# Performance work log

Measured on AMD Instinct MI355X. Metric: run time of the kernel, lower is better.

The kernel has to match this reference:

```python
import jax, jax.numpy as jnp
import numpy as np

N, E, F_IN, H, D, HID, G = 50000, 800000, 64, 4, 32, 128, 1024
NEG_SLOPE = 0.2


def setup_inputs():
    key = jax.random.key(0)
    ks = jax.random.split(key, 32)
    inp = {
        "x": jax.random.normal(ks[0], (N, F_IN), dtype=jnp.float32),
        "edge_index": jax.random.randint(ks[1], (2, E), 0, N, dtype=jnp.int64),
        "batch": jnp.sort(jax.random.randint(ks[2], (N,), 0, G, dtype=jnp.int64)),
    }
    dims = [F_IN, HID, HID]
    i = 3
    for l, din in enumerate(dims):
        s = 1.0 / np.sqrt(din)
        inp[f"Wl{l}"] = jax.random.normal(ks[i], (din, H * D), dtype=jnp.float32) * s; i += 1
        inp[f"bl{l}"] = jnp.zeros((H * D,), dtype=jnp.float32)
        inp[f"Wr{l}"] = jax.random.normal(ks[i], (din, H * D), dtype=jnp.float32) * s; i += 1
        inp[f"br{l}"] = jnp.zeros((H * D,), dtype=jnp.float32)
        inp[f"att{l}"] = jax.random.normal(ks[i], (H, D), dtype=jnp.float32) * (1.0 / np.sqrt(D)); i += 1
        inp[f"b{l}"] = jnp.zeros((H * D,), dtype=jnp.float32)
    inp["Wh"] = jax.random.normal(ks[i], (HID, 1), dtype=jnp.float32) * (1.0 / np.sqrt(HID))
    inp["bh"] = jnp.zeros((1,), dtype=jnp.float32)
    return inp


def gatv2_layer(x, src, dst, Wl, bl, Wr, br, att, b):
    # GATv2Conv (eval mode, no dropout): e_ij = att . leaky_relu(Wl x_j + Wr x_i)
    xl = (x @ Wl + bl).reshape(-1, H, D)   # source transform
    xr = (x @ Wr + br).reshape(-1, H, D)   # target transform
    m = xl[src] + xr[dst]                  # [E,H,D]
    e = jnp.where(m >= 0, m, NEG_SLOPE * m)
    score = jnp.einsum("ehd,hd->eh", e, att)          # [E,H]
    smax = jax.ops.segment_max(score, dst, num_segments=N)  # [N,H]
    expv = jnp.exp(score - smax[dst])
    denom = jax.ops.segment_sum(expv, dst, num_segments=N)
    alpha = expv / denom[dst]                          # softmax over in-edges of dst
    agg = jax.ops.segment_sum(alpha[:, :, None] * xl[src], dst, num_segments=N)
    return agg.reshape(-1, H * D) + b


def reference(x, edge_index, batch, Wl0, bl0, Wr0, br0, att0, b0,
              Wl1, bl1, Wr1, br1, att1, b1,
              Wl2, bl2, Wr2, br2, att2, b2, Wh, bh):
    src, dst = edge_index[0], edge_index[1]
    params = [(Wl0, bl0, Wr0, br0, att0, b0),
              (Wl1, bl1, Wr1, br1, att1, b1),
              (Wl2, bl2, Wr2, br2, att2, b2)]
    h = x
    for p in params:
        h = gatv2_layer(h, src, dst, *p)
        h = jax.nn.elu(h)  # dropout inactive in eval
    # global mean pool over graphs
    sums = jax.ops.segment_sum(h, batch, num_segments=G)
    cnt = jax.ops.segment_sum(jnp.ones((h.shape[0],), h.dtype), batch, num_segments=G)
    pooled = sums / jnp.maximum(cnt, 1.0)[:, None]
    return pooled @ Wh + bh
```

## Files before the change

kernel.cpp:

```cpp
#include <hip/hip_runtime.h>
#include <math.h>

#define N_NODES 50000
#define N_EDGES 800000
#define HD 128
#define GG 1024
#define NEG_SLOPE 0.2f
#define SCAN_B 1024
#define NB ((N_NODES + SCAN_B - 1) / SCAN_B)

typedef __attribute__((ext_vector_type(8))) short bf16x8;
typedef __attribute__((ext_vector_type(4))) float f32x4;

__device__ __forceinline__ unsigned short f2bf(float v) {
    unsigned u = __float_as_uint(v);
    u += 0x7fff + ((u >> 16) & 1);
    return (unsigned short)(u >> 16);
}
__device__ __forceinline__ float bf2f(unsigned short s) {
    return __uint_as_float((unsigned)s << 16);
}

__global__ void convert_x(const float* __restrict__ x, unsigned short* __restrict__ Xh,
                          unsigned short* __restrict__ Xl, int total)
{
    int i = blockIdx.x * 256 + threadIdx.x;
    if (i >= total) return;
    float v = x[i];
    unsigned short hi = f2bf(v);
    unsigned short lo = f2bf(v - bf2f(hi));
    Xh[i] = hi; Xl[i] = lo;
}

__global__ void convert_w(const float* __restrict__ Wl, const float* __restrict__ Wr,
                          unsigned short* __restrict__ Wth, unsigned short* __restrict__ Wtl,
                          int K)
{
    int t = blockIdx.x * 256 + threadIdx.x;
    if (t >= 256 * K) return;
    int c = t / K, k = t - c * K;
    float v = (c < 128) ? Wl[(size_t)k * 128 + c] : Wr[(size_t)k * 128 + (c - 128)];
    unsigned short hi = f2bf(v);
    unsigned short lo = f2bf(v - bf2f(hi));
    Wth[t] = hi; Wtl[t] = lo;
}

template<int K>
__launch_bounds__(256)
__global__ void gemm_mfma(const unsigned short* __restrict__ Xh, const unsigned short* __restrict__ Xl,
                          const unsigned short* __restrict__ Wth, const unsigned short* __restrict__ Wtl,
                          const float* __restrict__ bl, const float* __restrict__ br,
                          float* __restrict__ Cl, float* __restrict__ Cr, int n)
{
    constexpr int KC = 32;
    constexpr int NCH = K / KC;
    constexpr int XR = 40;
    __shared__ unsigned short XsH[64 * XR], XsL[64 * XR];
    __shared__ unsigned short WsH[256 * XR], WsL[256 * XR];
    const int tid  = threadIdx.x;
    const int wave = tid >> 6;
    const int lane = tid & 63;
    const int quad = lane >> 4;
    const int l15  = lane & 15;
    const int row0 = blockIdx.x * 64;

    f32x4 acc[4][4];
    #pragma unroll
    for (int i = 0; i < 4; i++)
        #pragma unroll
        for (int j = 0; j < 4; j++) acc[i][j] = (f32x4){0.f, 0.f, 0.f, 0.f};

    for (int ch = 0; ch < NCH; ch++) {
        const int k0 = ch * KC;
        {
            const int r = tid >> 2, seg = tid & 3;
            const int row = row0 + r;
            const size_t go = (size_t)row * K + k0 + seg * 8;
            uint4 vh = make_uint4(0, 0, 0, 0), vl = make_uint4(0, 0, 0, 0);
            if (row < n) { vh = *(const uint4*)(Xh + go); vl = *(const uint4*)(Xl + go); }
            *(uint4*)&XsH[r * XR + seg * 8] = vh;
            *(uint4*)&XsL[r * XR + seg * 8] = vl;
        }
        #pragma unroll
        for (int i = 0; i < 4; i++) {
            const int f = tid + i * 256;
            const int wr = f >> 2, seg = f & 3;
            const size_t go = (size_t)wr * K + k0 + seg * 8;
            *(uint4*)&WsH[wr * XR + seg * 8] = *(const uint4*)(Wth + go);
            *(uint4*)&WsL[wr * XR + seg * 8] = *(const uint4*)(Wtl + go);
        }
        __syncthreads();

        bf16x8 ah[4], al[4];
        #pragma unroll
        for (int mt = 0; mt < 4; mt++) {
            ah[mt] = *(const bf16x8*)&XsH[(mt * 16 + l15) * XR + quad * 8];
            al[mt] = *(const bf16x8*)&XsL[(mt * 16 + l15) * XR + quad * 8];
        }
        #pragma unroll
        for (int nt = 0; nt < 4; nt++) {
            const int wr = wave * 64 + nt * 16 + l15;
            const bf16x8 bh = *(const bf16x8*)&WsH[wr * XR + quad * 8];
            const bf16x8 bo = *(const bf16x8*)&WsL[wr * XR + quad * 8];
            #pragma unroll
            for (int mt = 0; mt < 4; mt++) {
                acc[mt][nt] = __builtin_amdgcn_mfma_f32_16x16x32_bf16(ah[mt], bh, acc[mt][nt], 0, 0, 0);
                acc[mt][nt] = __builtin_amdgcn_mfma_f32_16x16x32_bf16(ah[mt], bo, acc[mt][nt], 0, 0, 0);
                acc[mt][nt] = __builtin_amdgcn_mfma_f32_16x16x32_bf16(al[mt], bh, acc[mt][nt], 0, 0, 0);
            }
        }
        __syncthreads();
    }

    const bool isL = (wave < 2);
    const int colbase = (wave & 1) * 64;
    const float* bias = isL ? bl : br;
    float* C = isL ? Cl : Cr;
    #pragma unroll
    for (int nt = 0; nt < 4; nt++) {
        const float bv = bias[colbase + nt * 16 + l15];
        #pragma unroll
        for (int mt = 0; mt < 4; mt++) {
            #pragma unroll
            for (int r = 0; r < 4; r++) {
                const int row = row0 + mt * 16 + quad * 4 + r;
                if (row < n)
                    C[(size_t)row * 128 + colbase + nt * 16 + l15] = acc[mt][nt][r] + bv;
            }
        }
    }
}

__global__ void deg_hist(const int* __restrict__ dst, int* __restrict__ deg) {
    int e = blockIdx.x * 256 + threadIdx.x;
    if (e < N_EDGES) atomicAdd(&deg[dst[e]], 1);
}

__launch_bounds__(SCAN_B)
__global__ void scan_block(const int* __restrict__ deg, int* __restrict__ rowptr,
                           int* __restrict__ btot)
{
    __shared__ int s[SCAN_B];
    const int tid = threadIdx.x;
    const int i = blockIdx.x * SCAN_B + tid;
    int v = (i < N_NODES) ? deg[i] : 0;
    s[tid] = v;
    __syncthreads();
    for (int off = 1; off < SCAN_B; off <<= 1) {
        int t = (tid >= off) ? s[tid - off] : 0;
        __syncthreads();
        s[tid] += t;
        __syncthreads();
    }
    if (i < N_NODES) rowptr[i] = s[tid] - v;
    if (tid == SCAN_B - 1) btot[blockIdx.x] = s[SCAN_B - 1];
}

__global__ void scan_btot(const int* __restrict__ btot, int* __restrict__ boff) {
    if (threadIdx.x == 0) {
        int a = 0;
        for (int b = 0; b < NB; b++) { boff[b] = a; a += btot[b]; }
        boff[NB] = a;
    }
}

__global__ void scan_add(const int* __restrict__ boff, int* __restrict__ rowptr,
                         int* __restrict__ cursor)
{
    int i = blockIdx.x * 256 + threadIdx.x;
    if (i < N_NODES) {
        int r = rowptr[i] + boff[i >> 10];
        rowptr[i] = r;
        cursor[i] = r;
    }
    if (i == N_NODES) rowptr[N_NODES] = boff[NB];
}

__global__ void scatter_csr(const int* __restrict__ src, const int* __restrict__ dst,
                            int* __restrict__ cursor, int* __restrict__ csr_src)
{
    int e = blockIdx.x * 256 + threadIdx.x;
    if (e >= N_EDGES) return;
    int pos = atomicAdd(&cursor[dst[e]], 1);
    csr_src[pos] = src[e];
}

__global__ void build_gptr(const int* __restrict__ batch, int* __restrict__ gptr) {
    int i = blockIdx.x * 256 + threadIdx.x;
    if (i > N_NODES) return;
    if (i == 0) {
        for (int g = 0; g <= batch[0]; g++) gptr[g] = 0;
    } else if (i == N_NODES) {
        for (int g = batch[N_NODES - 1] + 1; g <= GG; g++) gptr[g] = N_NODES;
    } else {
        int b0 = batch[i - 1], b1 = batch[i];
        for (int g = b0 + 1; g <= b1; g++) gptr[g] = i;
    }
}

__launch_bounds__(256)
__global__ void node_attn(const float* __restrict__ xl, const float* __restrict__ xr,
                          const int* __restrict__ rowptr, const int* __restrict__ csr_src,
                          const float* __restrict__ att, const float* __restrict__ bvec,
                          unsigned short* __restrict__ Hh, unsigned short* __restrict__ Hl)
{
    const int node = (blockIdx.x * 256 + threadIdx.x) >> 6;
    const int lane = threadIdx.x & 63;
    if (node >= N_NODES) return;
    const int grp = lane >> 4;
    const int li  = lane & 15;

    const size_t nb = (size_t)node * HD + li * 8;
    const float4 xr0 = *(const float4*)(xr + nb);
    const float4 xr1 = *(const float4*)(xr + nb + 4);
    const float4 aw0 = *(const float4*)(att + li * 8);
    const float4 aw1 = *(const float4*)(att + li * 8 + 4);
    const int beg = rowptr[node];
    const int end = rowptr[node + 1];

    float m = -1e30f, l = 0.f;
    float4 a0 = make_float4(0.f, 0.f, 0.f, 0.f);
    float4 a1 = make_float4(0.f, 0.f, 0.f, 0.f);

    int e0 = beg + grp;
    int s0 = (e0 < end) ? csr_src[e0] : 0;
    float4 v0 = *(const float4*)(xl + (size_t)s0 * HD + li * 8);
    float4 v1 = *(const float4*)(xl + (size_t)s0 * HD + li * 8 + 4);

    for (int base = beg; base < end; base += 4) {
        const bool valid = (base + grp) < end;
        float4 n0 = v0, n1 = v1;
        if (base + 4 < end) {
            const int e2 = base + 4 + grp;
            const int s2 = (e2 < end) ? csr_src[e2] : 0;
            n0 = *(const float4*)(xl + (size_t)s2 * HD + li * 8);
            n1 = *(const float4*)(xl + (size_t)s2 * HD + li * 8 + 4);
        }
        float t, p;
        t = v0.x + xr0.x; t = fmaxf(t, NEG_SLOPE * t); p  = t * aw0.x;
        t = v0.y + xr0.y; t = fmaxf(t, NEG_SLOPE * t); p  = fmaf(t, aw0.y, p);
        t = v0.z + xr0.z; t = fmaxf(t, NEG_SLOPE * t); p  = fmaf(t, aw0.z, p);
        t = v0.w + xr0.w; t = fmaxf(t, NEG_SLOPE * t); p  = fmaf(t, aw0.w, p);
        t = v1.x + xr1.x; t = fmaxf(t, NEG_SLOPE * t); p  = fmaf(t, aw1.x, p);
        t = v1.y + xr1.y; t = fmaxf(t, NEG_SLOPE * t); p  = fmaf(t, aw1.y, p);
        t = v1.z + xr1.z; t = fmaxf(t, NEG_SLOPE * t); p  = fmaf(t, aw1.z, p);
        t = v1.w + xr1.w; t = fmaxf(t, NEG_SLOPE * t); p  = fmaf(t, aw1.w, p);
        p += __shfl_xor(p, 1);
        p += __shfl_xor(p, 2);

        const float mn = valid ? fmaxf(m, p) : m;
        const float w  = valid ? __expf(p - mn) : 0.f;
        const float sc = __expf(m - mn);
        l = fmaf(l, sc, w);
        a0.x = fmaf(a0.x, sc, w * v0.x);
        a0.y = fmaf(a0.y, sc, w * v0.y);
        a0.z = fmaf(a0.z, sc, w * v0.z);
        a0.w = fmaf(a0.w, sc, w * v0.w);
        a1.x = fmaf(a1.x, sc, w * v1.x);
        a1.y = fmaf(a1.y, sc, w * v1.y);
        a1.z = fmaf(a1.z, sc, w * v1.z);
        a1.w = fmaf(a1.w, sc, w * v1.w);
        m = mn;
        v0 = n0; v1 = n1;
    }

    #pragma unroll
    for (int off = 16; off < 64; off <<= 1) {
        const float mo = __shfl_xor(m, off);
        const float lo = __shfl_xor(l, off);
        float4 b0, b1;
        b0.x = __shfl_xor(a0.x, off); b0.y = __shfl_xor(a0.y, off);
        b0.z = __shfl_xor(a0.z, off); b0.w = __shfl_xor(a0.w, off);
        b1.x = __shfl_xor(a1.x, off); b1.y = __shfl_xor(a1.y, off);
        b1.z = __shfl_xor(a1.z, off); b1.w = __shfl_xor(a1.w, off);
        const float mm = fmaxf(m, mo);
        const float e1 = __expf(m - mm);
        const float e2 = __expf(mo - mm);
        l = l * e1 + lo * e2;
        a0.x = a0.x * e1 + b0.x * e2;
        a0.y = a0.y * e1 + b0.y * e2;
        a0.z = a0.z * e1 + b0.z * e2;
        a0.w = a0.w * e1 + b0.w * e2;
        a1.x = a1.x * e1 + b1.x * e2;
        a1.y = a1.y * e1 + b1.y * e2;
        a1.z = a1.z * e1 + b1.z * e2;
        a1.w = a1.w * e1 + b1.w * e2;
        m = mm;
    }

    if (grp == 0) {
        const float inv = (l > 0.f) ? 1.f / l : 0.f;
        const float4 bb0 = *(const float4*)(bvec + li * 8);
        const float4 bb1 = *(const float4*)(bvec + li * 8 + 4);
        float o[8];
        o[0] = fmaf(a0.x, inv, bb0.x);
        o[1] = fmaf(a0.y, inv, bb0.y);
        o[2] = fmaf(a0.z, inv, bb0.z);
        o[3] = fmaf(a0.w, inv, bb0.w);
        o[4] = fmaf(a1.x, inv, bb1.x);
        o[5] = fmaf(a1.y, inv, bb1.y);
        o[6] = fmaf(a1.z, inv, bb1.z);
        o[7] = fmaf(a1.w, inv, bb1.w);
        bf16x8 hv, lv;
        #pragma unroll
        for (int j = 0; j < 8; j++) {
            float e = (o[j] > 0.f) ? o[j] : expm1f(o[j]);
            unsigned short h = f2bf(e);
            hv[j] = (short)h;
            lv[j] = (short)f2bf(e - bf2f(h));
        }
        *(bf16x8*)(Hh + nb) = hv;
        *(bf16x8*)(Hl + nb) = lv;
    }
}

__launch_bounds__(256)
__global__ void pool_head(const unsigned short* __restrict__ Hh, const unsigned short* __restrict__ Hl,
                          const int* __restrict__ gptr, const float* __restrict__ Wh,
                          const float* __restrict__ bh, float* __restrict__ out)
{
    const int g = (blockIdx.x * 256 + threadIdx.x) >> 6;
    const int lane = threadIdx.x & 63;
    if (g >= GG) return;
    const int b0 = gptr[g], b1 = gptr[g + 1];
    const float2 w = *(const float2*)(Wh + lane * 2);
    float sx = 0.f, sy = 0.f;
    for (int i = b0; i < b1; i++) {
        const unsigned vh = *(const unsigned*)(Hh + (size_t)i * HD + lane * 2);
        const unsigned vl = *(const unsigned*)(Hl + (size_t)i * HD + lane * 2);
        sx += bf2f((unsigned short)(vh & 0xffff)) + bf2f((unsigned short)(vl & 0xffff));
        sy += bf2f((unsigned short)(vh >> 16))    + bf2f((unsigned short)(vl >> 16));
    }
    float d = sx * w.x + sy * w.y;
    d += __shfl_xor(d, 1);
    d += __shfl_xor(d, 2);
    d += __shfl_xor(d, 4);
    d += __shfl_xor(d, 8);
    d += __shfl_xor(d, 16);
    d += __shfl_xor(d, 32);
    if (lane == 0) out[g] = d / fmaxf((float)(b1 - b0), 1.f) + bh[0];
}

extern "C" void kernel_launch(void* const* d_in, const int* in_sizes, int n_in,
                              void* d_out, int out_size, void* d_ws, size_t ws_size,
                              hipStream_t stream)
{
    const float* x     = (const float*)d_in[0];
    const int*   edge  = (const int*)d_in[1];
    const int*   batch = (const int*)d_in[2];
    const int*   src   = edge;
    const int*   dst   = edge + N_EDGES;
    const float* Wh    = (const float*)d_in[21];
    const float* bh    = (const float*)d_in[22];
    float* out = (float*)d_out;

    const size_t N128 = (size_t)N_NODES * HD;
    float* buf_xl = (float*)d_ws;
    float* buf_xr = buf_xl + N128;
    unsigned short* Xh  = (unsigned short*)(buf_xr + N128);
    unsigned short* Xl_ = Xh + N128;
    unsigned short* Wth = Xl_ + N128;
    unsigned short* Wtl = Wth + 3 * 256 * 128;
    int* deg     = (int*)(Wtl + 3 * 256 * 128);
    int* rowptr  = deg + N_NODES;
    int* cursor  = rowptr + N_NODES + 1;
    int* csr_src = cursor + N_NODES;
    int* btot    = csr_src + N_EDGES;
    int* boff    = btot + NB;
    int* gptr    = boff + NB + 1;

    hipMemsetAsync(deg, 0, (size_t)N_NODES * sizeof(int), stream);
    deg_hist<<<(N_EDGES + 255) / 256, 256, 0, stream>>>(dst, deg);
    scan_block<<<NB, SCAN_B, 0, stream>>>(deg, rowptr, btot);
    scan_btot<<<1, 64, 0, stream>>>(btot, boff);
    scan_add<<<(N_NODES + 256) / 256, 256, 0, stream>>>(boff, rowptr, cursor);
    scatter_csr<<<(N_EDGES + 255) / 256, 256, 0, stream>>>(src, dst, cursor, csr_src);
    build_gptr<<<(N_NODES + 256) / 256, 256, 0, stream>>>(batch, gptr);

    convert_x<<<(N_NODES * 64 + 255) / 256, 256, 0, stream>>>(x, Xh, Xl_, N_NODES * 64);
    for (int l = 0; l < 3; l++) {
        const int K = (l == 0) ? 64 : 128;
        convert_w<<<(256 * K + 255) / 256, 256, 0, stream>>>(
            (const float*)d_in[3 + 6 * l], (const float*)d_in[5 + 6 * l],
            Wth + l * 256 * 128, Wtl + l * 256 * 128, K);
    }

    const int gemm_grid = (N_NODES + 63) / 64;
    const int attn_grid = (N_NODES + 3) / 4;

    for (int l = 0; l < 3; l++) {
        const float* bl  = (const float*)d_in[4 + 6 * l];
        const float* br  = (const float*)d_in[6 + 6 * l];
        const float* att = (const float*)d_in[7 + 6 * l];
        const float* bb  = (const float*)d_in[8 + 6 * l];

        if (l == 0)
            gemm_mfma<64><<<gemm_grid, 256, 0, stream>>>(Xh, Xl_, Wth, Wtl,
                                                         bl, br, buf_xl, buf_xr, N_NODES);
        else
            gemm_mfma<128><<<gemm_grid, 256, 0, stream>>>(Xh, Xl_,
                                                          Wth + l * 256 * 128, Wtl + l * 256 * 128,
                                                          bl, br, buf_xl, buf_xr, N_NODES);
        node_attn<<<attn_grid, 256, 0, stream>>>(buf_xl, buf_xr, rowptr, csr_src,
                                                 att, bb, Xh, Xl_);
    }

    pool_head<<<GG / 4, 256, 0, stream>>>(Xh, Xl_, gptr, Wh, bh, out);
}
```

Baseline: 516.2 us.

## Keep weights in registers for persistent GEMM, lazy softmax rescale, merge setup kernels

The GEMM becomes persistent: each wave holds a 32-column slice of the weight matrix in registers and loops over 64-row tiles, reading X straight from global memory with no LDS staging or barriers. The node attention folds log2(e) into the attention vector and uses exp2. It rescales the online-softmax accumulators only when some lane's score exceeds the running max by more than 8, which skips most rescale exponentials. Setup launches are merged: the three weight conversions become one kernel, and the block-total scan moves into scan_add via wave shuffles. Risks include higher register pressure, redundant global X loads across the 8 column waves, and lazy-max overflow if scores grow steadily in steps below the threshold.

```diff
diff --git a/kernel.cpp b/kernel.cpp
--- a/kernel.cpp
+++ b/kernel.cpp
@@ -8,6 +8,13 @@
 #define NEG_SLOPE 0.2f
 #define SCAN_B 1024
 #define NB ((N_NODES + SCAN_B - 1) / SCAN_B)
+#define LOG2E 1.4426950408889634f
+
+#if __has_builtin(__builtin_amdgcn_exp2f)
+#define EXP2F(x) __builtin_amdgcn_exp2f(x)
+#else
+#define EXP2F(x) exp2f(x)
+#endif
 
 typedef __attribute__((ext_vector_type(8))) short bf16x8;
 typedef __attribute__((ext_vector_type(4))) float f32x4;
@@ -32,102 +39,105 @@
     Xh[i] = hi; Xl[i] = lo;
 }
 
-__global__ void convert_w(const float* __restrict__ Wl, const float* __restrict__ Wr,
-                          unsigned short* __restrict__ Wth, unsigned short* __restrict__ Wtl,
-                          int K)
-{
-    int t = blockIdx.x * 256 + threadIdx.x;
-    if (t >= 256 * K) return;
-    int c = t / K, k = t - c * K;
-    float v = (c < 128) ? Wl[(size_t)k * 128 + c] : Wr[(size_t)k * 128 + (c - 128)];
-    unsigned short hi = f2bf(v);
-    unsigned short lo = f2bf(v - bf2f(hi));
-    Wth[t] = hi; Wtl[t] = lo;
+__global__ void convert_w_all(const float* __restrict__ W0l, const float* __restrict__ W0r,
+                              const float* __restrict__ W1l, const float* __restrict__ W1r,
+                              const float* __restrict__ W2l, const float* __restrict__ W2r,
+                              unsigned short* __restrict__ Wth, unsigned short* __restrict__ Wtl)
+{
+    const int t = blockIdx.x * 256 + threadIdx.x;
+    const float* Wl; const float* Wr;
+    int c, k, o;
+    if (t < 16384) {
+        c = t >> 6; k = t & 63; o = t;
+        Wl = W0l; Wr = W0r;
+    } else if (t < 49152) {
+        const int b = t - 16384; c = b >> 7; k = b & 127; o = 32768 + b;
+        Wl = W1l; Wr = W1r;
+    } else if (t < 81920) {
+        const int b = t - 49152; c = b >> 7; k = b & 127; o = 65536 + b;
+        Wl = W2l; Wr = W2r;
+    } else return;
+    const float v = (c < 128) ? Wl[(size_t)k * 128 + c] : Wr[(size_t)k * 128 + (c - 128)];
+    const unsigned short hi = f2bf(v);
+    Wth[o] = hi;
+    Wtl[o] = f2bf(v - bf2f(hi));
 }
 
 template<int K>
 __launch_bounds__(256)
-__global__ void gemm_mfma(const unsigned short* __restrict__ Xh, const unsigned short* __restrict__ Xl,
-                          const unsigned short* __restrict__ Wth, const unsigned short* __restrict__ Wtl,
-                          const float* __restrict__ bl, const float* __restrict__ br,
-                          float* __restrict__ Cl, float* __restrict__ Cr, int n)
-{
-    constexpr int KC = 32;
-    constexpr int NCH = K / KC;
-    constexpr int XR = 40;
-    __shared__ unsigned short XsH[64 * XR], XsL[64 * XR];
-    __shared__ unsigned short WsH[256 * XR], WsL[256 * XR];
+__global__ void gemm_reg(const unsigned short* __restrict__ Xh, const unsigned short* __restrict__ Xl,
+                         const unsigned short* __restrict__ Wth, const unsigned short* __restrict__ Wtl,
+                         const float* __restrict__ bl, const float* __restrict__ br,
+                         float* __restrict__ Cl, float* __restrict__ Cr, int n)
+{
+    constexpr int NCH = K / 32;
+    constexpr int RT  = (N_NODES + 63) / 64;
     const int tid  = threadIdx.x;
     const int wave = tid >> 6;
     const int lane = tid & 63;
     const int quad = lane >> 4;
     const int l15  = lane & 15;
-    const int row0 = blockIdx.x * 64;
-
-    f32x4 acc[4][4];
+    const int wid  = blockIdx.x * 4 + wave;
+    const int colid = wid & 7;
+    const int cb32  = colid * 32;
+    const int rs    = wid >> 3;
+    const int NS    = (gridDim.x * 4) >> 3;
+
+    bf16x8 Bh[NCH][2], Bo[NCH][2];
     #pragma unroll
-    for (int i = 0; i < 4; i++)
-        #pragma unroll
-        for (int j = 0; j < 4; j++) acc[i][j] = (f32x4){0.f, 0.f, 0.f, 0.f};
-
-    for (int ch = 0; ch < NCH; ch++) {
-        const int k0 = ch * KC;
-        {
-            const int r = tid >> 2, seg = tid & 3;
-            const int row = row0 + r;
-            const size_t go = (size_t)row * K + k0 + seg * 8;
-            uint4 vh = make_uint4(0, 0, 0, 0), vl = make_uint4(0, 0, 0, 0);
-            if (row < n) { vh = *(const uint4*)(Xh + go); vl = *(const uint4*)(Xl + go); }
-            *(uint4*)&XsH[r * XR + seg * 8] = vh;
-            *(uint4*)&XsL[r * XR + seg * 8] = vl;
-        }
-        #pragma unroll
-        for (int i = 0; i < 4; i++) {
-            const int f = tid + i * 256;
-            const int wr = f >> 2, seg = f & 3;
-            const size_t go = (size_t)wr * K + k0 + seg * 8;
-            *(uint4*)&WsH[wr * XR + seg * 8] = *(const uint4*)(Wth + go);
-            *(uint4*)&WsL[wr * XR + seg * 8] = *(const uint4*)(Wtl + go);
-        }
-        __syncthreads();
-
-        bf16x8 ah[4], al[4];
+    for (int ch = 0; ch < NCH; ch++)
+        #pragma unroll
+        for (int nt = 0; nt < 2; nt++) {
+            const size_t wo = (size_t)(cb32 + nt * 16 + l15) * K + ch * 32 + quad * 8;
+            Bh[ch][nt] = *(const bf16x8*)(Wth + wo);
+            Bo[ch][nt] = *(const bf16x8*)(Wtl + wo);
+        }
+
+    const int cb = cb32 & 127;
+    const float* bias = (colid < 4) ? bl : br;
+    float* C = (colid < 4) ? Cl : Cr;
+    float bv[2];
+    bv[0] = bias[cb + l15];
+    bv[1] = bias[cb + 16 + l15];
+
+    for (int rt = rs; rt < RT; rt += NS) {
+        const int row0 = rt * 64;
+        f32x4 acc[4][2];
         #pragma unroll
         for (int mt = 0; mt < 4; mt++) {
-            ah[mt] = *(const bf16x8*)&XsH[(mt * 16 + l15) * XR + quad * 8];
-            al[mt] = *(const bf16x8*)&XsL[(mt * 16 + l15) * XR + quad * 8];
-        }
-        #pragma unroll
-        for (int nt = 0; nt < 4; nt++) {
-            const int wr = wave * 64 + nt * 16 + l15;
-            const bf16x8 bh = *(const bf16x8*)&WsH[wr * XR + quad * 8];
-            const bf16x8 bo = *(const bf16x8*)&WsL[wr * XR + quad * 8];
+            acc[mt][0] = (f32x4){0.f, 0.f, 0.f, 0.f};
+            acc[mt][1] = (f32x4){0.f, 0.f, 0.f, 0.f};
+        }
+        #pragma unroll
+        for (int ch = 0; ch < NCH; ch++) {
+            bf16x8 ah[4], al[4];
             #pragma unroll
             for (int mt = 0; mt < 4; mt++) {
-                acc[mt][nt] = __builtin_amdgcn_mfma_f32_16x16x32_bf16(ah[mt], bh, acc[mt][nt], 0, 0, 0);
-                acc[mt][nt] = __builtin_amdgcn_mfma_f32_16x16x32_bf16(ah[mt], bo, acc[mt][nt], 0, 0, 0);
-                acc[mt][nt] = __builtin_amdgcn_mfma_f32_16x16x32_bf16(al[mt], bh, acc[mt][nt], 0, 0, 0);
+                int r = row0 + mt * 16 + l15;
+                r = (r < n) ? r : (n - 1);
+                const size_t go = (size_t)r * K + ch * 32 + quad * 8;
+                ah[mt] = *(const bf16x8*)(Xh + go);
+                al[mt] = *(const bf16x8*)(Xl + go);
             }
-        }
-        __syncthreads();
-    }
-
-    const bool isL = (wave < 2);
-    const int colbase = (wave & 1) * 64;
-    const float* bias = isL ? bl : br;
-    float* C = isL ? Cl : Cr;
-    #pragma unroll
-    for (int nt = 0; nt < 4; nt++) {
-        const float bv = bias[colbase + nt * 16 + l15];
-        #pragma unroll
-        for (int mt = 0; mt < 4; mt++) {
             #pragma unroll
-            for (int r = 0; r < 4; r++) {
-                const int row = row0 + mt * 16 + quad * 4 + r;
-                if (row < n)
-                    C[(size_t)row * 128 + colbase + nt * 16 + l15] = acc[mt][nt][r] + bv;
-            }
-        }
+            for (int nt = 0; nt < 2; nt++)
+                #pragma unroll
+                for (int mt = 0; mt < 4; mt++) {
+                    acc[mt][nt] = __builtin_amdgcn_mfma_f32_16x16x32_bf16(ah[mt], Bh[ch][nt], acc[mt][nt], 0, 0, 0);
+                    acc[mt][nt] = __builtin_amdgcn_mfma_f32_16x16x32_bf16(ah[mt], Bo[ch][nt], acc[mt][nt], 0, 0, 0);
+                    acc[mt][nt] = __builtin_amdgcn_mfma_f32_16x16x32_bf16(al[mt], Bh[ch][nt], acc[mt][nt], 0, 0, 0);
+                }
+        }
+        #pragma unroll
+        for (int nt = 0; nt < 2; nt++)
+            #pragma unroll
+            for (int mt = 0; mt < 4; mt++)
+                #pragma unroll
+                for (int r = 0; r < 4; r++) {
+                    const int row = row0 + mt * 16 + quad * 4 + r;
+                    if (row < n)
+                        C[(size_t)row * 128 + cb + nt * 16 + l15] = acc[mt][nt][r] + bv[nt];
+                }
     }
 }
 
@@ -156,24 +166,31 @@
     if (tid == SCAN_B - 1) btot[blockIdx.x] = s[SCAN_B - 1];
 }
 
-__global__ void scan_btot(const int* __restrict__ btot, int* __restrict__ boff) {
-    if (threadIdx.x == 0) {
-        int a = 0;
-        for (int b = 0; b < NB; b++) { boff[b] = a; a += btot[b]; }
-        boff[NB] = a;
-    }
-}
-
-__global__ void scan_add(const int* __restrict__ boff, int* __restrict__ rowptr,
+__launch_bounds__(256)
+__global__ void scan_add(const int* __restrict__ btot, int* __restrict__ rowptr,
                          int* __restrict__ cursor)
 {
-    int i = blockIdx.x * 256 + threadIdx.x;
+    __shared__ int sb[NB + 1];
+    const int tid = threadIdx.x;
+    if (tid < 64) {
+        const int v = (tid < NB) ? btot[tid] : 0;
+        int incl = v;
+        #pragma unroll
+        for (int off = 1; off < 64; off <<= 1) {
+            const int t = __shfl_up(incl, off);
+            if (tid >= off) incl += t;
+        }
+        if (tid < NB) sb[tid] = incl - v;
+        if (tid == NB - 1) sb[NB] = incl;
+    }
+    __syncthreads();
+    const int i = blockIdx.x * 256 + tid;
     if (i < N_NODES) {
-        int r = rowptr[i] + boff[i >> 10];
+        const int r = rowptr[i] + sb[i >> 10];
         rowptr[i] = r;
         cursor[i] = r;
     }
-    if (i == N_NODES) rowptr[N_NODES] = boff[NB];
+    if (i == N_NODES) rowptr[N_NODES] = sb[NB];
 }
 
 __global__ void scatter_csr(const int* __restrict__ src, const int* __restrict__ dst,
@@ -213,8 +230,10 @@
     const size_t nb = (size_t)node * HD + li * 8;
     const float4 xr0 = *(const float4*)(xr + nb);
     const float4 xr1 = *(const float4*)(xr + nb + 4);
-    const float4 aw0 = *(const float4*)(att + li * 8);
-    const float4 aw1 = *(const float4*)(att + li * 8 + 4);
+    float4 aw0 = *(const float4*)(att + li * 8);
+    float4 aw1 = *(const float4*)(att + li * 8 + 4);
+    aw0.x *= LOG2E; aw0.y *= LOG2E; aw0.z *= LOG2E; aw0.w *= LOG2E;
+    aw1.x *= LOG2E; aw1.y *= LOG2E; aw1.z *= LOG2E; aw1.w *= LOG2E;
     const int beg = rowptr[node];
     const int end = rowptr[node + 1];
 
@@ -248,19 +267,33 @@
         p += __shfl_xor(p, 1);
         p += __shfl_xor(p, 2);
 
-        const float mn = valid ? fmaxf(m, p) : m;
-        const float w  = valid ? __expf(p - mn) : 0.f;
-        const float sc = __expf(m - mn);
-        l = fmaf(l, sc, w);
-        a0.x = fmaf(a0.x, sc, w * v0.x);
-        a0.y = fmaf(a0.y, sc, w * v0.y);
-        a0.z = fmaf(a0.z, sc, w * v0.z);
-        a0.w = fmaf(a0.w, sc, w * v0.w);
-        a1.x = fmaf(a1.x, sc, w * v1.x);
-        a1.y = fmaf(a1.y, sc, w * v1.y);
-        a1.z = fmaf(a1.z, sc, w * v1.z);
-        a1.w = fmaf(a1.w, sc, w * v1.w);
-        m = mn;
+        const bool grow = valid && (p > m + 8.f);
+        if (__any(grow)) {
+            const float mn = valid ? fmaxf(m, p) : m;
+            const float sc = EXP2F(m - mn);
+            const float w  = valid ? EXP2F(p - mn) : 0.f;
+            l = fmaf(l, sc, w);
+            a0.x = fmaf(a0.x, sc, w * v0.x);
+            a0.y = fmaf(a0.y, sc, w * v0.y);
+            a0.z = fmaf(a0.z, sc, w * v0.z);
+            a0.w = fmaf(a0.w, sc, w * v0.w);
+            a1.x = fmaf(a1.x, sc, w * v1.x);
+            a1.y = fmaf(a1.y, sc, w * v1.y);
+            a1.z = fmaf(a1.z, sc, w * v1.z);
+            a1.w = fmaf(a1.w, sc, w * v1.w);
+            m = mn;
+        } else {
+            const float w = valid ? EXP2F(p - m) : 0.f;
+            l += w;
+            a0.x = fmaf(w, v0.x, a0.x);
+            a0.y = fmaf(w, v0.y, a0.y);
+            a0.z = fmaf(w, v0.z, a0.z);
+            a0.w = fmaf(w, v0.w, a0.w);
+            a1.x = fmaf(w, v1.x, a1.x);
+            a1.y = fmaf(w, v1.y, a1.y);
+            a1.z = fmaf(w, v1.z, a1.z);
+            a1.w = fmaf(w, v1.w, a1.w);
+        }
         v0 = n0; v1 = n1;
     }
 
@@ -274,8 +307,8 @@
         b1.x = __shfl_xor(a1.x, off); b1.y = __shfl_xor(a1.y, off);
         b1.z = __shfl_xor(a1.z, off); b1.w = __shfl_xor(a1.w, off);
         const float mm = fmaxf(m, mo);
-        const float e1 = __expf(m - mm);
-        const float e2 = __expf(mo - mm);
+        const float e1 = EXP2F(m - mm);
+        const float e2 = EXP2F(mo - mm);
         l = l * e1 + lo * e2;
         a0.x = a0.x * e1 + b0.x * e2;
         a0.y = a0.y * e1 + b0.y * e2;
@@ -372,20 +405,18 @@
     hipMemsetAsync(deg, 0, (size_t)N_NODES * sizeof(int), stream);
     deg_hist<<<(N_EDGES + 255) / 256, 256, 0, stream>>>(dst, deg);
     scan_block<<<NB, SCAN_B, 0, stream>>>(deg, rowptr, btot);
-    scan_btot<<<1, 64, 0, stream>>>(btot, boff);
-    scan_add<<<(N_NODES + 256) / 256, 256, 0, stream>>>(boff, rowptr, cursor);
+    scan_add<<<(N_NODES + 256) / 256, 256, 0, stream>>>(btot, rowptr, cursor);
     scatter_csr<<<(N_EDGES + 255) / 256, 256, 0, stream>>>(src, dst, cursor, csr_src);
     build_gptr<<<(N_NODES + 256) / 256, 256, 0, stream>>>(batch, gptr);
 
     convert_x<<<(N_NODES * 64 + 255) / 256, 256, 0, stream>>>(x, Xh, Xl_, N_NODES * 64);
-    for (int l = 0; l < 3; l++) {
-        const int K = (l == 0) ? 64 : 128;
-        convert_w<<<(256 * K + 255) / 256, 256, 0, stream>>>(
-            (const float*)d_in[3 + 6 * l], (const float*)d_in[5 + 6 * l],
-            Wth + l * 256 * 128, Wtl + l * 256 * 128, K);
-    }
-
-    const int gemm_grid = (N_NODES + 63) / 64;
+    convert_w_all<<<320, 256, 0, stream>>>(
+        (const float*)d_in[3], (const float*)d_in[5],
+        (const float*)d_in[9], (const float*)d_in[11],
+        (const float*)d_in[15], (const float*)d_in[17],
+        Wth, Wtl);
+
+    const int gemm_grid = 768;
     const int attn_grid = (N_NODES + 3) / 4;
 
     for (int l = 0; l < 3; l++) {
@@ -395,12 +426,12 @@
         const float* bb  = (const float*)d_in[8 + 6 * l];
 
         if (l == 0)
-            gemm_mfma<64><<<gemm_grid, 256, 0, stream>>>(Xh, Xl_, Wth, Wtl,
+            gemm_reg<64><<<gemm_grid, 256, 0, stream>>>(Xh, Xl_, Wth, Wtl,
+                                                        bl, br, buf_xl, buf_xr, N_NODES);
+        else
+            gemm_reg<128><<<gemm_grid, 256, 0, stream>>>(Xh, Xl_,
+                                                         Wth + l * 256 * 128, Wtl + l * 256 * 128,
                                                          bl, br, buf_xl, buf_xr, N_NODES);
-        else
-            gemm_mfma<128><<<gemm_grid, 256, 0, stream>>>(Xh, Xl_,
-                                                          Wth + l * 256 * 128, Wtl + l * 256 * 128,
-                                                          bl, br, buf_xl, buf_xr, N_NODES);
         node_attn<<<attn_grid, 256, 0, stream>>>(buf_xl, buf_xr, rowptr, csr_src,
                                                  att, bb, Xh, Xl_);
     }
```

New measurement: 514.2 us. Within noise of the previous version (-0.4%).
